# Performance work log

Hardware: AMD Instinct MI355X
Metric: run time of the kernel (lower is better)

The kernel has to match this reference:

```python
import jax, jax.numpy as jnp
import numpy as np


def setup_inputs() -> dict:
    key = jax.random.key(0)
    k1, k2, k3, k4, k5 = jax.random.split(key, 5)
    B, S, H, F, E = 2, 512, 1024, 3584, 8
    scale_in = 1.0 / np.sqrt(H)
    scale_ff = 1.0 / np.sqrt(F)
    return {
        "hidden_states": jax.random.normal(k1, (B, S, H), dtype=jnp.float32),
        "gate_w": jax.random.normal(k2, (E, H), dtype=jnp.float32) * scale_in,
        "w1": jax.random.normal(k3, (E, F, H), dtype=jnp.float32) * scale_in,
        "w2": jax.random.normal(k4, (E, H, F), dtype=jnp.float32) * scale_ff,
        "w3": jax.random.normal(k5, (E, F, H), dtype=jnp.float32) * scale_in,
    }


TOP_K = 2


def reference(hidden_states, gate_w, w1, w2, w3):
    B, S, H = hidden_states.shape
    E = gate_w.shape[0]
    x = hidden_states.reshape(B * S, H)  # [T, H]
    T = x.shape[0]

    # Router: softmax in fp32, top-2 selection, renormalize selected weights.
    router_logits = x @ gate_w.T  # [T, E]
    probs = jax.nn.softmax(router_logits.astype(jnp.float32), axis=-1)
    top_vals, top_idx = jax.lax.top_k(probs, TOP_K)  # [T, K]
    top_vals = top_vals / jnp.sum(top_vals, axis=-1, keepdims=True)
    top_vals = top_vals.astype(x.dtype)

    # Dense routing-weight matrix [T, E]: weight if selected else 0
    # (equivalent to the one-hot expert_mask + index_add combine).
    dense_w = jnp.zeros((T, E), dtype=x.dtype).at[
        jnp.arange(T)[:, None], top_idx
    ].add(top_vals)

    # Expert SwiGLU MLPs, batched over the expert axis.
    h1 = jnp.einsum("th,efh->etf", x, w1)  # [E, T, F]
    h3 = jnp.einsum("th,efh->etf", x, w3)  # [E, T, F]
    y = jnp.einsum("etf,ehf->eth", jax.nn.silu(h1) * h3, w2)  # [E, T, H]

    # Weighted combine across experts.
    out = jnp.einsum("eth,te->th", y, dense_w)  # [T, H]
    return out.reshape(B, S, H), router_logits
```

## Files before the change

kernel.cpp:

```cpp
#include <hip/hip_runtime.h>
#include <hip/hip_bf16.h>

typedef __bf16 v8bf __attribute__((ext_vector_type(8)));
typedef __bf16 v4bf __attribute__((ext_vector_type(4)));
typedef float  f32x4 __attribute__((ext_vector_type(4)));
typedef unsigned int u32;

#define NTOK 1024
#define HDIM 1024
#define FDIM 3584
#define NEXP 8
#define NPAIR 2048
#define MAXT 16
#define KSPLIT2 4
#define KPER2 (FDIM / KSPLIT2)

#define OFF_COUNTS   0
#define OFF_OFFSETS  64
#define OFF_NT1      128
#define OFF_T1E      192
#define OFF_T1M      320
#define OFF_TOKIDX   2048
#define OFF_TOKWT    (2048 + 4*NPAIR)
#define OFF_PAIRTOK  (OFF_TOKWT + 4*NPAIR)
#define OFF_PAIRWT   (OFF_PAIRTOK + 4*NPAIR)
#define OFF_SLOTOF   (OFF_PAIRWT + 4*NPAIR)
#define OFF_XB       65536
#define OFF_ACT      (OFF_XB + 2ull*NTOK*HDIM)
#define OFF_Y        (OFF_ACT + 2ull*NPAIR*FDIM)
#define YSTRIDE      ((size_t)NPAIR * HDIM)

static __device__ inline v4bf cvt4(float4 f) {
    v4bf r;
    r[0] = (__bf16)f.x; r[1] = (__bf16)f.y; r[2] = (__bf16)f.z; r[3] = (__bf16)f.w;
    return r;
}

static __device__ inline v8bf pack8(f32x4 lo, f32x4 hi) {
    v8bf r;
    r[0] = (__bf16)lo[0]; r[1] = (__bf16)lo[1]; r[2] = (__bf16)lo[2]; r[3] = (__bf16)lo[3];
    r[4] = (__bf16)hi[0]; r[5] = (__bf16)hi[1]; r[6] = (__bf16)hi[2]; r[7] = (__bf16)hi[3];
    return r;
}

#define FENCE() asm volatile("" ::: "memory")
#define BARRIER() do { FENCE(); __builtin_amdgcn_s_barrier(); FENCE(); } while (0)
#define WAITVM0() asm volatile("s_waitcnt vmcnt(0)" ::: "memory")
#define WAITLGKM0() asm volatile("s_waitcnt lgkmcnt(0)" ::: "memory")

#define DMA16(SRC, DST) \
    __builtin_amdgcn_global_load_lds((const __attribute__((address_space(1))) u32*)(SRC), \
                                     (__attribute__((address_space(3))) u32*)(DST), 16, 0, 0)

__global__ __launch_bounds__(256) void moe_cvtx(const float* __restrict__ x,
                                                __bf16* __restrict__ xb)
{
    const size_t i = ((size_t)blockIdx.x * 256 + threadIdx.x) * 4;
    float4 v = *(const float4*)(x + i);
    *(v4bf*)(xb + i) = cvt4(v);
}

__global__ __launch_bounds__(256) void moe_router(
    const float* __restrict__ x, const float* __restrict__ gw,
    float* __restrict__ logits, int* __restrict__ counts,
    int* __restrict__ tok_idx, float* __restrict__ tok_wt)
{
    const int lane = threadIdx.x & 63;
    const int wv = threadIdx.x >> 6;
    const int t = blockIdx.x * 4 + wv;
    const float* xr = x + (size_t)t * HDIM;

    float acc[NEXP];
#pragma unroll
    for (int e = 0; e < NEXP; ++e) acc[e] = 0.f;
#pragma unroll
    for (int j = 0; j < 4; ++j) {
        int h = lane * 4 + j * 256;
        float4 xv = *(const float4*)(xr + h);
#pragma unroll
        for (int e = 0; e < NEXP; ++e) {
            float4 g = *(const float4*)(gw + e * HDIM + h);
            acc[e] += xv.x * g.x + xv.y * g.y + xv.z * g.z + xv.w * g.w;
        }
    }
#pragma unroll
    for (int e = 0; e < NEXP; ++e) {
#pragma unroll
        for (int s = 32; s > 0; s >>= 1) acc[e] += __shfl_xor(acc[e], s);
    }
    if (lane == 0) {
#pragma unroll
        for (int e = 0; e < NEXP; ++e) logits[t * NEXP + e] = acc[e];
        int i0 = 0;
#pragma unroll
        for (int e = 1; e < NEXP; ++e) if (acc[e] > acc[i0]) i0 = e;
        int i1 = (i0 == 0) ? 1 : 0;
#pragma unroll
        for (int e = 0; e < NEXP; ++e) if (e != i0 && acc[e] > acc[i1]) i1 = e;
        float w0 = 1.f / (1.f + expf(acc[i1] - acc[i0]));
        float w1 = 1.f - w0;
        tok_idx[2 * t] = i0; tok_idx[2 * t + 1] = i1;
        tok_wt[2 * t] = w0;  tok_wt[2 * t + 1] = w1;
        atomicAdd(&counts[i0], 1);
        atomicAdd(&counts[i1], 1);
    }
}

__global__ void moe_scatter(const int* __restrict__ counts, const int* __restrict__ tok_idx,
                            const float* __restrict__ tok_wt, int* __restrict__ offsets,
                            int* __restrict__ pair_token, float* __restrict__ pair_wt,
                            int* __restrict__ slot_of,
                            int* __restrict__ t1e, int* __restrict__ t1m, int* __restrict__ nt1)
{
    __shared__ int cur[NEXP];
    const int tid = threadIdx.x;
    if (tid == 0) {
        int run = 0, n1 = 0;
        for (int e = 0; e < NEXP; ++e) {
            offsets[e] = run; cur[e] = run;
            for (int m0 = 0; m0 < counts[e]; m0 += 256) { t1e[n1] = e; t1m[n1] = m0; ++n1; }
            run += counts[e];
        }
        *nt1 = n1;
    }
    __syncthreads();
    for (int p = tid; p < 2 * NTOK; p += blockDim.x) {
        int e = tok_idx[p];
        int s = atomicAdd(&cur[e], 1);
        pair_token[s] = p >> 1;
        pair_wt[s] = tok_wt[p];
        slot_of[p] = s;
    }
}

__global__ __launch_bounds__(256, 2) void moe_gemm1(
    const __bf16* __restrict__ xb, const float* __restrict__ w1g,
    const float* __restrict__ w3g, const int* __restrict__ counts,
    const int* __restrict__ offsets, const int* __restrict__ pair_token,
    const int* __restrict__ t1e, const int* __restrict__ t1m,
    const int* __restrict__ nt1,
    __bf16* __restrict__ act)
{
    const int ty = blockIdx.y;
    if (ty >= *nt1) return;
    const int e = t1e[ty];
    const int m0 = t1m[ty];
    const int Me = counts[e];
    const int rows = min(256, Me - m0);
    const int slot0 = offsets[e] + m0;
    const int n0 = blockIdx.x * 32;

    __shared__ __align__(16) __bf16 As[256 * 64];
    __shared__ __align__(16) float  B1s[32 * 64];
    __shared__ __align__(16) float  B3s[32 * 64];

    const int tid = threadIdx.x;
    const int lane = tid & 63;
    const int wv = tid >> 6;
    const int ln4 = lane >> 4;
    const int lr = lane & 15;
    const int wm = (wv >> 1) * 128;
    const int wn = (wv & 1) * 16;

    f32x4 acc1[8], acc3[8];
#pragma unroll
    for (int i = 0; i < 8; ++i) {
        acc1[i] = (f32x4){0.f, 0.f, 0.f, 0.f};
        acc3[i] = (f32x4){0.f, 0.f, 0.f, 0.f};
    }

    const char* asrc[8];
#pragma unroll
    for (int i = 0; i < 8; ++i) {
        int c = i * 256 + tid;
        int r = c >> 3;
        int rr = (r < rows) ? r : 0;
        int sj = (c & 7) ^ (r & 7);
        asrc[i] = (const char*)(xb + (size_t)pair_token[slot0 + rr] * HDIM) + sj * 16;
    }
    const char* bsrc[2];
#pragma unroll
    for (int i = 0; i < 2; ++i) {
        int c = i * 256 + tid;
        int r = c >> 4;
        int sj = (c & 15) ^ (r & 15);
        bsrc[i] = (const char*)(w1g + ((size_t)e * FDIM + n0 + r) * HDIM) + sj * 16;
    }
    const ptrdiff_t d31b = (const char*)w3g - (const char*)w1g;

#define DMA_ALL1(K0) do { \
    _Pragma("unroll") \
    for (int i = 0; i < 8; ++i) \
        DMA16(asrc[i] + (size_t)(K0) * 128, (char*)As + (i * 256 + wv * 64) * 16); \
    _Pragma("unroll") \
    for (int i = 0; i < 2; ++i) { \
        DMA16(bsrc[i] + (size_t)(K0) * 256,        (char*)B1s + (i * 256 + wv * 64) * 16); \
        DMA16(bsrc[i] + d31b + (size_t)(K0) * 256, (char*)B3s + (i * 256 + wv * 64) * 16); \
    } } while (0)

    int abase[8], axor[8];
#pragma unroll
    for (int i = 0; i < 8; ++i) {
        int row = wm + i * 16 + lr;
        abase[i] = row * 128;
        axor[i] = (row & 7) << 4;
    }
    int bbase, bxor;
    {
        int row = wn + lr;
        bbase = row * 256;
        bxor = (row & 15) << 4;
    }

#define CMP1() do { \
    _Pragma("unroll") \
    for (int ksub = 0; ksub < 2; ++ksub) { \
        int in0 = ksub * 128 + ln4 * 32; \
        v8bf b1f = pack8(*(const f32x4*)((const char*)B1s + bbase + ((in0) ^ bxor)), \
                         *(const f32x4*)((const char*)B1s + bbase + ((in0 + 16) ^ bxor))); \
        v8bf b3f = pack8(*(const f32x4*)((const char*)B3s + bbase + ((in0) ^ bxor)), \
                         *(const f32x4*)((const char*)B3s + bbase + ((in0 + 16) ^ bxor))); \
        _Pragma("unroll") \
        for (int mi = 0; mi < 8; ++mi) { \
            v8bf af = *(const v8bf*)((const char*)As + abase[mi] + ((ksub * 64 + ln4 * 16) ^ axor[mi])); \
            acc1[mi] = __builtin_amdgcn_mfma_f32_16x16x32_bf16(af, b1f, acc1[mi], 0, 0, 0); \
            acc3[mi] = __builtin_amdgcn_mfma_f32_16x16x32_bf16(af, b3f, acc3[mi], 0, 0, 0); \
        } } } while (0)

    DMA_ALL1(0);
    for (int ks = 0; ks < HDIM / 64; ++ks) {
        WAITVM0();
        BARRIER();
        CMP1();
        WAITLGKM0();
        BARRIER();
        if (ks + 1 < HDIM / 64) DMA_ALL1(ks + 1);
    }
#undef DMA_ALL1
#undef CMP1

    const int rj = ln4 * 4;
#pragma unroll
    for (int mi = 0; mi < 8; ++mi) {
#pragma unroll
        for (int j = 0; j < 4; ++j) {
            int rm = wm + mi * 16 + rj + j;
            if (rm < rows) {
                size_t rowoff = (size_t)(slot0 + rm) * FDIM + n0 + wn;
                float h1 = acc1[mi][j];
                float h3 = acc3[mi][j];
                float sv = (h1 / (1.f + __expf(-h1))) * h3;
                act[rowoff + lr] = (__bf16)sv;
            }
        }
    }
}

__global__ __launch_bounds__(256, 2) void moe_gemm2(
    const __bf16* __restrict__ act, const float* __restrict__ w2g,
    const int* __restrict__ counts, const int* __restrict__ offsets,
    const int* __restrict__ t1e, const int* __restrict__ t1m,
    const int* __restrict__ nt1,
    float* __restrict__ y)
{
    const int ty = blockIdx.y;
    if (ty >= *nt1) return;
    const int e = t1e[ty];
    const int m0 = t1m[ty];
    const int Me = counts[e];
    const int rows = min(256, Me - m0);
    const int slot0 = offsets[e] + m0;
    const int n0 = blockIdx.x * 64;
    const int kz = blockIdx.z;
    float* yout = y + (size_t)kz * YSTRIDE;
    const size_t kbase = (size_t)kz * KPER2;

    __shared__ __align__(16) __bf16 As[256 * 64];
    __shared__ __align__(16) float  Bs[64 * 64];

    const int tid = threadIdx.x;
    const int lane = tid & 63;
    const int wv = tid >> 6;
    const int ln4 = lane >> 4;
    const int lr = lane & 15;
    const int wm = (wv >> 1) * 128;
    const int wn = (wv & 1) * 32;

    f32x4 acc[8][2];
#pragma unroll
    for (int i = 0; i < 8; ++i)
#pragma unroll
        for (int j = 0; j < 2; ++j) acc[i][j] = (f32x4){0.f, 0.f, 0.f, 0.f};

    const char* asrc[8];
#pragma unroll
    for (int i = 0; i < 8; ++i) {
        int c = i * 256 + tid;
        int r = c >> 3;
        int rr = (r < rows) ? r : 0;
        int sj = (c & 7) ^ (r & 7);
        asrc[i] = (const char*)(act + (size_t)(slot0 + rr) * FDIM + kbase) + sj * 16;
    }
    const char* bsrc[4];
#pragma unroll
    for (int i = 0; i < 4; ++i) {
        int c = i * 256 + tid;
        int r = c >> 4;
        int sj = (c & 15) ^ (r & 15);
        bsrc[i] = (const char*)(w2g + ((size_t)e * HDIM + n0 + r) * FDIM + kbase) + sj * 16;
    }

#define DMA_ALL2(K0) do { \
    _Pragma("unroll") \
    for (int i = 0; i < 8; ++i) \
        DMA16(asrc[i] + (size_t)(K0) * 128, (char*)As + (i * 256 + wv * 64) * 16); \
    _Pragma("unroll") \
    for (int i = 0; i < 4; ++i) \
        DMA16(bsrc[i] + (size_t)(K0) * 256, (char*)Bs + (i * 256 + wv * 64) * 16); \
    } while (0)

    int abase[8], axor[8];
#pragma unroll
    for (int i = 0; i < 8; ++i) {
        int row = wm + i * 16 + lr;
        abase[i] = row * 128;
        axor[i] = (row & 7) << 4;
    }
    int bbase[2], bxor[2];
#pragma unroll
    for (int i = 0; i < 2; ++i) {
        int row = wn + i * 16 + lr;
        bbase[i] = row * 256;
        bxor[i] = (row & 15) << 4;
    }

#define CMP2() do { \
    _Pragma("unroll") \
    for (int ksub = 0; ksub < 2; ++ksub) { \
        v8bf bf[2]; \
        _Pragma("unroll") \
        for (int ni = 0; ni < 2; ++ni) { \
            int in0 = ksub * 128 + ln4 * 32; \
            bf[ni] = pack8(*(const f32x4*)((const char*)Bs + bbase[ni] + ((in0) ^ bxor[ni])), \
                           *(const f32x4*)((const char*)Bs + bbase[ni] + ((in0 + 16) ^ bxor[ni]))); } \
        _Pragma("unroll") \
        for (int mi = 0; mi < 8; ++mi) { \
            v8bf af = *(const v8bf*)((const char*)As + abase[mi] + ((ksub * 64 + ln4 * 16) ^ axor[mi])); \
            _Pragma("unroll") \
            for (int ni = 0; ni < 2; ++ni) \
                acc[mi][ni] = __builtin_amdgcn_mfma_f32_16x16x32_bf16(af, bf[ni], acc[mi][ni], 0, 0, 0); \
        } } } while (0)

    DMA_ALL2(0);
    for (int ks = 0; ks < KPER2 / 64; ++ks) {
        WAITVM0();
        BARRIER();
        CMP2();
        WAITLGKM0();
        BARRIER();
        if (ks + 1 < KPER2 / 64) DMA_ALL2(ks + 1);
    }
#undef DMA_ALL2
#undef CMP2

    const int rj = ln4 * 4;
#pragma unroll
    for (int mi = 0; mi < 8; ++mi) {
#pragma unroll
        for (int j = 0; j < 4; ++j) {
            int rm = wm + mi * 16 + rj + j;
            if (rm < rows) {
                size_t rowoff = (size_t)(slot0 + rm) * HDIM + n0 + wn;
#pragma unroll
                for (int ni = 0; ni < 2; ++ni)
                    yout[rowoff + ni * 16 + lr] = acc[mi][ni][j];
            }
        }
    }
}

__global__ __launch_bounds__(256) void moe_combine(
    const float* __restrict__ y, const int* __restrict__ slot_of,
    const float* __restrict__ pair_wt, float* __restrict__ out)
{
    const int t = blockIdx.x;
    const int tid = threadIdx.x;
    const int s0 = slot_of[2 * t];
    const int s1 = slot_of[2 * t + 1];
    const float w0 = pair_wt[s0];
    const float w1 = pair_wt[s1];
    float4 a = {0.f, 0.f, 0.f, 0.f}, b = {0.f, 0.f, 0.f, 0.f};
#pragma unroll
    for (int k = 0; k < KSPLIT2; ++k) {
        const float4 ak = *(const float4*)(y + k * YSTRIDE + (size_t)s0 * HDIM + tid * 4);
        const float4 bk = *(const float4*)(y + k * YSTRIDE + (size_t)s1 * HDIM + tid * 4);
        a.x += ak.x; a.y += ak.y; a.z += ak.z; a.w += ak.w;
        b.x += bk.x; b.y += bk.y; b.z += bk.z; b.w += bk.w;
    }
    float4 o;
    o.x = w0 * a.x + w1 * b.x;
    o.y = w0 * a.y + w1 * b.y;
    o.z = w0 * a.z + w1 * b.z;
    o.w = w0 * a.w + w1 * b.w;
    *(float4*)(out + (size_t)t * HDIM + tid * 4) = o;
}

extern "C" void kernel_launch(void* const* d_in, const int* in_sizes, int n_in,
                              void* d_out, int out_size, void* d_ws, size_t ws_size,
                              hipStream_t stream) {
    const float* x   = (const float*)d_in[0];
    const float* gw  = (const float*)d_in[1];
    const float* w1  = (const float*)d_in[2];
    const float* w2  = (const float*)d_in[3];
    const float* w3  = (const float*)d_in[4];

    float* out    = (float*)d_out;
    float* logits = out + (size_t)NTOK * HDIM;

    char* ws = (char*)d_ws;
    int*    counts     = (int*)(ws + OFF_COUNTS);
    int*    offsets    = (int*)(ws + OFF_OFFSETS);
    int*    nt1        = (int*)(ws + OFF_NT1);
    int*    t1e        = (int*)(ws + OFF_T1E);
    int*    t1m        = (int*)(ws + OFF_T1M);
    int*    tok_idx    = (int*)(ws + OFF_TOKIDX);
    float*  tok_wt     = (float*)(ws + OFF_TOKWT);
    int*    pair_token = (int*)(ws + OFF_PAIRTOK);
    float*  pair_wt    = (float*)(ws + OFF_PAIRWT);
    int*    slot_of    = (int*)(ws + OFF_SLOTOF);
    __bf16* xb         = (__bf16*)(ws + OFF_XB);
    __bf16* act        = (__bf16*)(ws + OFF_ACT);
    float*  yb         = (float*)(ws + OFF_Y);

    hipMemsetAsync(counts, 0, 64, stream);

    moe_cvtx<<<dim3(NTOK * HDIM / 1024), dim3(256), 0, stream>>>(x, xb);
    moe_router<<<dim3(NTOK / 4), dim3(256), 0, stream>>>(x, gw, logits, counts, tok_idx, tok_wt);
    moe_scatter<<<dim3(1), dim3(256), 0, stream>>>(counts, tok_idx, tok_wt, offsets,
                                                   pair_token, pair_wt, slot_of,
                                                   t1e, t1m, nt1);
    moe_gemm1<<<dim3(FDIM / 32, MAXT), dim3(256), 0, stream>>>(
        xb, w1, w3, counts, offsets, pair_token, t1e, t1m, nt1, act);
    moe_gemm2<<<dim3(HDIM / 64, MAXT, KSPLIT2), dim3(256), 0, stream>>>(
        act, w2, counts, offsets, t1e, t1m, nt1, yb);
    moe_combine<<<dim3(NTOK), dim3(256), 0, stream>>>(yb, slot_of, pair_wt, out);
}
```

Measured before the change: 192.1 us.

## Double-buffer MoE GEMM smem tiles and shrink M tiles to 128 rows

Both expert GEMMs now keep two shared-memory buffers and prefetch two K-steps ahead. They wait with partial vmcnt counts, so global-to-LDS DMA overlaps the MFMA work, and they raise wave priority around the compute. Token tiles shrink from 256 to 128 rows, which doubles the maximum tile count. GEMM2 uses 32-wide N tiles, a K-split of 2 and a higher occupancy bound, so more blocks are in flight and latency is better hidden. The risk is that the fp32 expert weights are re-read by twice as many M tiles, which adds memory traffic unless L2 absorbs it.

```diff
diff --git a/kernel.cpp b/kernel.cpp
--- a/kernel.cpp
+++ b/kernel.cpp
@@ -11,9 +11,11 @@
 #define FDIM 3584
 #define NEXP 8
 #define NPAIR 2048
-#define MAXT 16
-#define KSPLIT2 4
+#define MAXT 32
+#define KSPLIT2 2
 #define KPER2 (FDIM / KSPLIT2)
+#define NS1 (HDIM / 64)
+#define NS2 (KPER2 / 64)
 
 #define OFF_COUNTS   0
 #define OFF_OFFSETS  64
@@ -45,7 +47,7 @@
 
 #define FENCE() asm volatile("" ::: "memory")
 #define BARRIER() do { FENCE(); __builtin_amdgcn_s_barrier(); FENCE(); } while (0)
-#define WAITVM0() asm volatile("s_waitcnt vmcnt(0)" ::: "memory")
+#define WAITVM(N) asm volatile("s_waitcnt vmcnt(" #N ")" ::: "memory")
 #define WAITLGKM0() asm volatile("s_waitcnt lgkmcnt(0)" ::: "memory")
 
 #define DMA16(SRC, DST) \
@@ -118,7 +120,7 @@
         int run = 0, n1 = 0;
         for (int e = 0; e < NEXP; ++e) {
             offsets[e] = run; cur[e] = run;
-            for (int m0 = 0; m0 < counts[e]; m0 += 256) { t1e[n1] = e; t1m[n1] = m0; ++n1; }
+            for (int m0 = 0; m0 < counts[e]; m0 += 128) { t1e[n1] = e; t1m[n1] = m0; ++n1; }
             run += counts[e];
         }
         *nt1 = n1;
@@ -146,32 +148,32 @@
     const int e = t1e[ty];
     const int m0 = t1m[ty];
     const int Me = counts[e];
-    const int rows = min(256, Me - m0);
+    const int rows = min(128, Me - m0);
     const int slot0 = offsets[e] + m0;
     const int n0 = blockIdx.x * 32;
 
-    __shared__ __align__(16) __bf16 As[256 * 64];
-    __shared__ __align__(16) float  B1s[32 * 64];
-    __shared__ __align__(16) float  B3s[32 * 64];
+    __shared__ __align__(16) __bf16 As[2][128 * 64];
+    __shared__ __align__(16) float  B1s[2][32 * 64];
+    __shared__ __align__(16) float  B3s[2][32 * 64];
 
     const int tid = threadIdx.x;
     const int lane = tid & 63;
     const int wv = tid >> 6;
     const int ln4 = lane >> 4;
     const int lr = lane & 15;
-    const int wm = (wv >> 1) * 128;
+    const int wm = (wv >> 1) * 64;
     const int wn = (wv & 1) * 16;
 
-    f32x4 acc1[8], acc3[8];
-#pragma unroll
-    for (int i = 0; i < 8; ++i) {
+    f32x4 acc1[4], acc3[4];
+#pragma unroll
+    for (int i = 0; i < 4; ++i) {
         acc1[i] = (f32x4){0.f, 0.f, 0.f, 0.f};
         acc3[i] = (f32x4){0.f, 0.f, 0.f, 0.f};
     }
 
-    const char* asrc[8];
-#pragma unroll
-    for (int i = 0; i < 8; ++i) {
+    const char* asrc[4];
+#pragma unroll
+    for (int i = 0; i < 4; ++i) {
         int c = i * 256 + tid;
         int r = c >> 3;
         int rr = (r < rows) ? r : 0;
@@ -188,19 +190,19 @@
     }
     const ptrdiff_t d31b = (const char*)w3g - (const char*)w1g;
 
-#define DMA_ALL1(K0) do { \
-    _Pragma("unroll") \
-    for (int i = 0; i < 8; ++i) \
-        DMA16(asrc[i] + (size_t)(K0) * 128, (char*)As + (i * 256 + wv * 64) * 16); \
+#define DMA1(BUF, K0) do { \
+    _Pragma("unroll") \
+    for (int i = 0; i < 4; ++i) \
+        DMA16(asrc[i] + (size_t)(K0) * 128, (char*)&As[BUF][0] + (i * 256 + wv * 64) * 16); \
     _Pragma("unroll") \
     for (int i = 0; i < 2; ++i) { \
-        DMA16(bsrc[i] + (size_t)(K0) * 256,        (char*)B1s + (i * 256 + wv * 64) * 16); \
-        DMA16(bsrc[i] + d31b + (size_t)(K0) * 256, (char*)B3s + (i * 256 + wv * 64) * 16); \
+        DMA16(bsrc[i] + (size_t)(K0) * 256,        (char*)&B1s[BUF][0] + (i * 256 + wv * 64) * 16); \
+        DMA16(bsrc[i] + d31b + (size_t)(K0) * 256, (char*)&B3s[BUF][0] + (i * 256 + wv * 64) * 16); \
     } } while (0)
 
-    int abase[8], axor[8];
-#pragma unroll
-    for (int i = 0; i < 8; ++i) {
+    int abase[4], axor[4];
+#pragma unroll
+    for (int i = 0; i < 4; ++i) {
         int row = wm + i * 16 + lr;
         abase[i] = row * 128;
         axor[i] = (row & 7) << 4;
@@ -212,51 +214,58 @@
         bxor = (row & 15) << 4;
     }
 
-#define CMP1() do { \
+#define CMP1(BUF) do { \
+    const char* Ab = (const char*)&As[BUF][0]; \
+    const char* B1b = (const char*)&B1s[BUF][0]; \
+    const char* B3b = (const char*)&B3s[BUF][0]; \
+    __builtin_amdgcn_s_setprio(1); \
     _Pragma("unroll") \
     for (int ksub = 0; ksub < 2; ++ksub) { \
         int in0 = ksub * 128 + ln4 * 32; \
-        v8bf b1f = pack8(*(const f32x4*)((const char*)B1s + bbase + ((in0) ^ bxor)), \
-                         *(const f32x4*)((const char*)B1s + bbase + ((in0 + 16) ^ bxor))); \
-        v8bf b3f = pack8(*(const f32x4*)((const char*)B3s + bbase + ((in0) ^ bxor)), \
-                         *(const f32x4*)((const char*)B3s + bbase + ((in0 + 16) ^ bxor))); \
+        v8bf b1f = pack8(*(const f32x4*)(B1b + bbase + ((in0) ^ bxor)), \
+                         *(const f32x4*)(B1b + bbase + ((in0 + 16) ^ bxor))); \
+        v8bf b3f = pack8(*(const f32x4*)(B3b + bbase + ((in0) ^ bxor)), \
+                         *(const f32x4*)(B3b + bbase + ((in0 + 16) ^ bxor))); \
         _Pragma("unroll") \
-        for (int mi = 0; mi < 8; ++mi) { \
-            v8bf af = *(const v8bf*)((const char*)As + abase[mi] + ((ksub * 64 + ln4 * 16) ^ axor[mi])); \
+        for (int mi = 0; mi < 4; ++mi) { \
+            v8bf af = *(const v8bf*)(Ab + abase[mi] + ((ksub * 64 + ln4 * 16) ^ axor[mi])); \
             acc1[mi] = __builtin_amdgcn_mfma_f32_16x16x32_bf16(af, b1f, acc1[mi], 0, 0, 0); \
             acc3[mi] = __builtin_amdgcn_mfma_f32_16x16x32_bf16(af, b3f, acc3[mi], 0, 0, 0); \
-        } } } while (0)
-
-    DMA_ALL1(0);
-    for (int ks = 0; ks < HDIM / 64; ++ks) {
-        WAITVM0();
+        } } \
+    __builtin_amdgcn_s_setprio(0); \
+    } while (0)
+
+    DMA1(0, 0);
+    DMA1(1, 1);
+    for (int ks = 0; ks < NS1; ++ks) {
+        if (ks < NS1 - 1) WAITVM(8);
+        else              WAITVM(0);
         BARRIER();
-        CMP1();
+        CMP1(ks & 1);
         WAITLGKM0();
         BARRIER();
-        if (ks + 1 < HDIM / 64) DMA_ALL1(ks + 1);
-    }
-#undef DMA_ALL1
+        if (ks + 2 < NS1) DMA1(ks & 1, ks + 2);
+    }
+#undef DMA1
 #undef CMP1
 
     const int rj = ln4 * 4;
 #pragma unroll
-    for (int mi = 0; mi < 8; ++mi) {
+    for (int mi = 0; mi < 4; ++mi) {
 #pragma unroll
         for (int j = 0; j < 4; ++j) {
             int rm = wm + mi * 16 + rj + j;
             if (rm < rows) {
-                size_t rowoff = (size_t)(slot0 + rm) * FDIM + n0 + wn;
                 float h1 = acc1[mi][j];
                 float h3 = acc3[mi][j];
                 float sv = (h1 / (1.f + __expf(-h1))) * h3;
-                act[rowoff + lr] = (__bf16)sv;
+                act[(size_t)(slot0 + rm) * FDIM + n0 + wn + lr] = (__bf16)sv;
             }
         }
     }
 }
 
-__global__ __launch_bounds__(256, 2) void moe_gemm2(
+__global__ __launch_bounds__(256, 3) void moe_gemm2(
     const __bf16* __restrict__ act, const float* __restrict__ w2g,
     const int* __restrict__ counts, const int* __restrict__ offsets,
     const int* __restrict__ t1e, const int* __restrict__ t1m,
@@ -268,112 +277,108 @@
     const int e = t1e[ty];
     const int m0 = t1m[ty];
     const int Me = counts[e];
-    const int rows = min(256, Me - m0);
+    const int rows = min(128, Me - m0);
     const int slot0 = offsets[e] + m0;
-    const int n0 = blockIdx.x * 64;
+    const int n0 = blockIdx.x * 32;
     const int kz = blockIdx.z;
     float* yout = y + (size_t)kz * YSTRIDE;
     const size_t kbase = (size_t)kz * KPER2;
 
-    __shared__ __align__(16) __bf16 As[256 * 64];
-    __shared__ __align__(16) float  Bs[64 * 64];
+    __shared__ __align__(16) __bf16 As[2][128 * 64];
+    __shared__ __align__(16) float  Bs[2][32 * 64];
 
     const int tid = threadIdx.x;
     const int lane = tid & 63;
     const int wv = tid >> 6;
     const int ln4 = lane >> 4;
     const int lr = lane & 15;
-    const int wm = (wv >> 1) * 128;
-    const int wn = (wv & 1) * 32;
-
-    f32x4 acc[8][2];
-#pragma unroll
-    for (int i = 0; i < 8; ++i)
-#pragma unroll
-        for (int j = 0; j < 2; ++j) acc[i][j] = (f32x4){0.f, 0.f, 0.f, 0.f};
-
-    const char* asrc[8];
-#pragma unroll
-    for (int i = 0; i < 8; ++i) {
+    const int wm = (wv >> 1) * 64;
+    const int wn = (wv & 1) * 16;
+
+    f32x4 acc[4];
+#pragma unroll
+    for (int i = 0; i < 4; ++i) acc[i] = (f32x4){0.f, 0.f, 0.f, 0.f};
+
+    const char* asrc[4];
+#pragma unroll
+    for (int i = 0; i < 4; ++i) {
         int c = i * 256 + tid;
         int r = c >> 3;
         int rr = (r < rows) ? r : 0;
         int sj = (c & 7) ^ (r & 7);
         asrc[i] = (const char*)(act + (size_t)(slot0 + rr) * FDIM + kbase) + sj * 16;
     }
-    const char* bsrc[4];
-#pragma unroll
-    for (int i = 0; i < 4; ++i) {
+    const char* bsrc[2];
+#pragma unroll
+    for (int i = 0; i < 2; ++i) {
         int c = i * 256 + tid;
         int r = c >> 4;
         int sj = (c & 15) ^ (r & 15);
         bsrc[i] = (const char*)(w2g + ((size_t)e * HDIM + n0 + r) * FDIM + kbase) + sj * 16;
     }
 
-#define DMA_ALL2(K0) do { \
-    _Pragma("unroll") \
-    for (int i = 0; i < 8; ++i) \
-        DMA16(asrc[i] + (size_t)(K0) * 128, (char*)As + (i * 256 + wv * 64) * 16); \
+#define DMA2(BUF, K0) do { \
     _Pragma("unroll") \
     for (int i = 0; i < 4; ++i) \
-        DMA16(bsrc[i] + (size_t)(K0) * 256, (char*)Bs + (i * 256 + wv * 64) * 16); \
+        DMA16(asrc[i] + (size_t)(K0) * 128, (char*)&As[BUF][0] + (i * 256 + wv * 64) * 16); \
+    _Pragma("unroll") \
+    for (int i = 0; i < 2; ++i) \
+        DMA16(bsrc[i] + (size_t)(K0) * 256, (char*)&Bs[BUF][0] + (i * 256 + wv * 64) * 16); \
     } while (0)
 
-    int abase[8], axor[8];
-#pragma unroll
-    for (int i = 0; i < 8; ++i) {
+    int abase[4], axor[4];
+#pragma unroll
+    for (int i = 0; i < 4; ++i) {
         int row = wm + i * 16 + lr;
         abase[i] = row * 128;
         axor[i] = (row & 7) << 4;
     }
-    int bbase[2], bxor[2];
-#pragma unroll
-    for (int i = 0; i < 2; ++i) {
-        int row = wn + i * 16 + lr;
-        bbase[i] = row * 256;
-        bxor[i] = (row & 15) << 4;
-    }
-
-#define CMP2() do { \
+    int bbase, bxor;
+    {
+        int row = wn + lr;
+        bbase = row * 256;
+        bxor = (row & 15) << 4;
+    }
+
+#define CMP2(BUF) do { \
+    const char* Ab = (const char*)&As[BUF][0]; \
+    const char* Bb = (const char*)&Bs[BUF][0]; \
+    __builtin_amdgcn_s_setprio(1); \
     _Pragma("unroll") \
     for (int ksub = 0; ksub < 2; ++ksub) { \
-        v8bf bf[2]; \
+        int in0 = ksub * 128 + ln4 * 32; \
+        v8bf bf = pack8(*(const f32x4*)(Bb + bbase + ((in0) ^ bxor)), \
+                        *(const f32x4*)(Bb + bbase + ((in0 + 16) ^ bxor))); \
         _Pragma("unroll") \
-        for (int ni = 0; ni < 2; ++ni) { \
-            int in0 = ksub * 128 + ln4 * 32; \
-            bf[ni] = pack8(*(const f32x4*)((const char*)Bs + bbase[ni] + ((in0) ^ bxor[ni])), \
-                           *(const f32x4*)((const char*)Bs + bbase[ni] + ((in0 + 16) ^ bxor[ni]))); } \
-        _Pragma("unroll") \
-        for (int mi = 0; mi < 8; ++mi) { \
-            v8bf af = *(const v8bf*)((const char*)As + abase[mi] + ((ksub * 64 + ln4 * 16) ^ axor[mi])); \
-            _Pragma("unroll") \
-            for (int ni = 0; ni < 2; ++ni) \
-                acc[mi][ni] = __builtin_amdgcn_mfma_f32_16x16x32_bf16(af, bf[ni], acc[mi][ni], 0, 0, 0); \
-        } } } while (0)
-
-    DMA_ALL2(0);
-    for (int ks = 0; ks < KPER2 / 64; ++ks) {
-        WAITVM0();
+        for (int mi = 0; mi < 4; ++mi) { \
+            v8bf af = *(const v8bf*)(Ab + abase[mi] + ((ksub * 64 + ln4 * 16) ^ axor[mi])); \
+            acc[mi] = __builtin_amdgcn_mfma_f32_16x16x32_bf16(af, bf, acc[mi], 0, 0, 0); \
+        } } \
+    __builtin_amdgcn_s_setprio(0); \
+    } while (0)
+
+    DMA2(0, 0);
+    DMA2(1, 1);
+    for (int ks = 0; ks < NS2; ++ks) {
+        if (ks < NS2 - 1) WAITVM(6);
+        else              WAITVM(0);
         BARRIER();
-        CMP2();
+        CMP2(ks & 1);
         WAITLGKM0();
         BARRIER();
-        if (ks + 1 < KPER2 / 64) DMA_ALL2(ks + 1);
-    }
-#undef DMA_ALL2
+        if (ks + 2 < NS2) DMA2(ks & 1, ks + 2);
+    }
+#undef DMA2
 #undef CMP2
 
     const int rj = ln4 * 4;
 #pragma unroll
-    for (int mi = 0; mi < 8; ++mi) {
+    for (int mi = 0; mi < 4; ++mi) {
 #pragma unroll
         for (int j = 0; j < 4; ++j) {
             int rm = wm + mi * 16 + rj + j;
             if (rm < rows) {
-                size_t rowoff = (size_t)(slot0 + rm) * HDIM + n0 + wn;
-#pragma unroll
-                for (int ni = 0; ni < 2; ++ni)
-                    yout[rowoff + ni * 16 + lr] = acc[mi][ni][j];
+                yout[(size_t)(slot0 + rm) * HDIM + n0 + wn + lr] = acc[mi][j];
             }
         }
     }
@@ -441,7 +446,7 @@
                                                    t1e, t1m, nt1);
     moe_gemm1<<<dim3(FDIM / 32, MAXT), dim3(256), 0, stream>>>(
         xb, w1, w3, counts, offsets, pair_token, t1e, t1m, nt1, act);
-    moe_gemm2<<<dim3(HDIM / 64, MAXT, KSPLIT2), dim3(256), 0, stream>>>(
+    moe_gemm2<<<dim3(HDIM / 32, MAXT, KSPLIT2), dim3(256), 0, stream>>>(
         act, w2, counts, offsets, t1e, t1m, nt1, yb);
     moe_combine<<<dim3(NTOK), dim3(256), 0, stream>>>(yb, slot_of, pair_wt, out);
 }
```

Result: slower. 212.1 us (+10.4%).

## Fuse MoE combine into gemm2 via atomics, smaller M tiles, XCD-aware block swizzle

Applied to the files above, without the earlier changes.

Drops the separate combine kernel and the fp32 split-K partial buffer. gemm2 now multiplies each result by its routing weight and atomically adds it straight into the zeroed output. gemm2 uses 128-row M tiles with a separate tile list, occupancy of 4, and loads all A and B fragments before the MFMAs. Both GEMMs use a 1D grid with an 8-way XCD swizzle so blocks that share weights land on the same XCD. This removes a large intermediate write and read plus one launch, at the cost of fp32 atomic contention, non-deterministic summation order, and an extra memset of the output.

```diff
diff --git a/kernel.cpp b/kernel.cpp
--- a/kernel.cpp
+++ b/kernel.cpp
@@ -11,15 +11,28 @@
 #define FDIM 3584
 #define NEXP 8
 #define NPAIR 2048
-#define MAXT 16
+#define MAXT1 16
+#define MAXT2 32
 #define KSPLIT2 4
 #define KPER2 (FDIM / KSPLIT2)
+#define NS1 (HDIM / 64)
+#define NS2 (KPER2 / 64)
+
+#define G1_NB (FDIM / 32)
+#define G1_NWG (G1_NB * MAXT1)
+#define G1_CPX (G1_NWG / 8)
+#define G2_NB (HDIM / 64)
+#define G2_NWG (G2_NB * KSPLIT2 * MAXT2)
+#define G2_CPX (G2_NWG / 8)
 
 #define OFF_COUNTS   0
 #define OFF_OFFSETS  64
 #define OFF_NT1      128
+#define OFF_NT2      132
 #define OFF_T1E      192
 #define OFF_T1M      320
+#define OFF_T2E      448
+#define OFF_T2M      704
 #define OFF_TOKIDX   2048
 #define OFF_TOKWT    (2048 + 4*NPAIR)
 #define OFF_PAIRTOK  (OFF_TOKWT + 4*NPAIR)
@@ -27,8 +40,6 @@
 #define OFF_SLOTOF   (OFF_PAIRWT + 4*NPAIR)
 #define OFF_XB       65536
 #define OFF_ACT      (OFF_XB + 2ull*NTOK*HDIM)
-#define OFF_Y        (OFF_ACT + 2ull*NPAIR*FDIM)
-#define YSTRIDE      ((size_t)NPAIR * HDIM)
 
 static __device__ inline v4bf cvt4(float4 f) {
     v4bf r;
@@ -110,18 +121,20 @@
                             const float* __restrict__ tok_wt, int* __restrict__ offsets,
                             int* __restrict__ pair_token, float* __restrict__ pair_wt,
                             int* __restrict__ slot_of,
-                            int* __restrict__ t1e, int* __restrict__ t1m, int* __restrict__ nt1)
+                            int* __restrict__ t1e, int* __restrict__ t1m, int* __restrict__ nt1,
+                            int* __restrict__ t2e, int* __restrict__ t2m, int* __restrict__ nt2)
 {
     __shared__ int cur[NEXP];
     const int tid = threadIdx.x;
     if (tid == 0) {
-        int run = 0, n1 = 0;
+        int run = 0, n1 = 0, n2 = 0;
         for (int e = 0; e < NEXP; ++e) {
             offsets[e] = run; cur[e] = run;
             for (int m0 = 0; m0 < counts[e]; m0 += 256) { t1e[n1] = e; t1m[n1] = m0; ++n1; }
+            for (int m0 = 0; m0 < counts[e]; m0 += 128) { t2e[n2] = e; t2m[n2] = m0; ++n2; }
             run += counts[e];
         }
-        *nt1 = n1;
+        *nt1 = n1; *nt2 = n2;
     }
     __syncthreads();
     for (int p = tid; p < 2 * NTOK; p += blockDim.x) {
@@ -141,14 +154,17 @@
     const int* __restrict__ nt1,
     __bf16* __restrict__ act)
 {
-    const int ty = blockIdx.y;
+    const int g = blockIdx.x;
+    const int swz = (g & 7) * G1_CPX + (g >> 3);
+    const int ty = swz % MAXT1;
+    const int nb = swz / MAXT1;
     if (ty >= *nt1) return;
     const int e = t1e[ty];
     const int m0 = t1m[ty];
     const int Me = counts[e];
     const int rows = min(256, Me - m0);
     const int slot0 = offsets[e] + m0;
-    const int n0 = blockIdx.x * 32;
+    const int n0 = nb * 32;
 
     __shared__ __align__(16) __bf16 As[256 * 64];
     __shared__ __align__(16) float  B1s[32 * 64];
@@ -228,13 +244,13 @@
         } } } while (0)
 
     DMA_ALL1(0);
-    for (int ks = 0; ks < HDIM / 64; ++ks) {
+    for (int ks = 0; ks < NS1; ++ks) {
         WAITVM0();
         BARRIER();
         CMP1();
         WAITLGKM0();
         BARRIER();
-        if (ks + 1 < HDIM / 64) DMA_ALL1(ks + 1);
+        if (ks + 1 < NS1) DMA_ALL1(ks + 1);
     }
 #undef DMA_ALL1
 #undef CMP1
@@ -256,26 +272,30 @@
     }
 }
 
-__global__ __launch_bounds__(256, 2) void moe_gemm2(
+__global__ __launch_bounds__(256, 4) void moe_gemm2(
     const __bf16* __restrict__ act, const float* __restrict__ w2g,
     const int* __restrict__ counts, const int* __restrict__ offsets,
-    const int* __restrict__ t1e, const int* __restrict__ t1m,
-    const int* __restrict__ nt1,
-    float* __restrict__ y)
+    const int* __restrict__ pair_token, const float* __restrict__ pair_wt,
+    const int* __restrict__ t2e, const int* __restrict__ t2m,
+    const int* __restrict__ nt2,
+    float* __restrict__ out)
 {
-    const int ty = blockIdx.y;
-    if (ty >= *nt1) return;
-    const int e = t1e[ty];
-    const int m0 = t1m[ty];
+    const int g = blockIdx.x;
+    const int swz = (g & 7) * G2_CPX + (g >> 3);
+    const int ty = swz % MAXT2;
+    const int rest = swz / MAXT2;
+    const int kz = rest % KSPLIT2;
+    const int nb = rest / KSPLIT2;
+    if (ty >= *nt2) return;
+    const int e = t2e[ty];
+    const int m0 = t2m[ty];
     const int Me = counts[e];
-    const int rows = min(256, Me - m0);
+    const int rows = min(128, Me - m0);
     const int slot0 = offsets[e] + m0;
-    const int n0 = blockIdx.x * 64;
-    const int kz = blockIdx.z;
-    float* yout = y + (size_t)kz * YSTRIDE;
+    const int n0 = nb * 64;
     const size_t kbase = (size_t)kz * KPER2;
 
-    __shared__ __align__(16) __bf16 As[256 * 64];
+    __shared__ __align__(16) __bf16 As[128 * 64];
     __shared__ __align__(16) float  Bs[64 * 64];
 
     const int tid = threadIdx.x;
@@ -283,18 +303,18 @@
     const int wv = tid >> 6;
     const int ln4 = lane >> 4;
     const int lr = lane & 15;
-    const int wm = (wv >> 1) * 128;
+    const int wm = (wv >> 1) * 64;
     const int wn = (wv & 1) * 32;
 
-    f32x4 acc[8][2];
-#pragma unroll
-    for (int i = 0; i < 8; ++i)
+    f32x4 acc[4][2];
+#pragma unroll
+    for (int i = 0; i < 4; ++i)
 #pragma unroll
         for (int j = 0; j < 2; ++j) acc[i][j] = (f32x4){0.f, 0.f, 0.f, 0.f};
 
-    const char* asrc[8];
-#pragma unroll
-    for (int i = 0; i < 8; ++i) {
+    const char* asrc[4];
+#pragma unroll
+    for (int i = 0; i < 4; ++i) {
         int c = i * 256 + tid;
         int r = c >> 3;
         int rr = (r < rows) ? r : 0;
@@ -310,18 +330,15 @@
         bsrc[i] = (const char*)(w2g + ((size_t)e * HDIM + n0 + r) * FDIM + kbase) + sj * 16;
     }
 
-#define DMA_ALL2(K0) do { \
-    _Pragma("unroll") \
-    for (int i = 0; i < 8; ++i) \
+#define DMA_ALL2(K0) do { _Pragma("unroll") \
+    for (int i = 0; i < 4; ++i) { \
         DMA16(asrc[i] + (size_t)(K0) * 128, (char*)As + (i * 256 + wv * 64) * 16); \
-    _Pragma("unroll") \
-    for (int i = 0; i < 4; ++i) \
         DMA16(bsrc[i] + (size_t)(K0) * 256, (char*)Bs + (i * 256 + wv * 64) * 16); \
-    } while (0)
-
-    int abase[8], axor[8];
-#pragma unroll
-    for (int i = 0; i < 8; ++i) {
+    } } while (0)
+
+    int abase[4], axor[4];
+#pragma unroll
+    for (int i = 0; i < 4; ++i) {
         int row = wm + i * 16 + lr;
         abase[i] = row * 128;
         axor[i] = (row & 7) << 4;
@@ -335,74 +352,54 @@
     }
 
 #define CMP2() do { \
-    _Pragma("unroll") \
-    for (int ksub = 0; ksub < 2; ++ksub) { \
-        v8bf bf[2]; \
-        _Pragma("unroll") \
-        for (int ni = 0; ni < 2; ++ni) { \
-            int in0 = ksub * 128 + ln4 * 32; \
-            bf[ni] = pack8(*(const f32x4*)((const char*)Bs + bbase[ni] + ((in0) ^ bxor[ni])), \
-                           *(const f32x4*)((const char*)Bs + bbase[ni] + ((in0 + 16) ^ bxor[ni]))); } \
-        _Pragma("unroll") \
-        for (int mi = 0; mi < 8; ++mi) { \
-            v8bf af = *(const v8bf*)((const char*)As + abase[mi] + ((ksub * 64 + ln4 * 16) ^ axor[mi])); \
-            _Pragma("unroll") \
-            for (int ni = 0; ni < 2; ++ni) \
-                acc[mi][ni] = __builtin_amdgcn_mfma_f32_16x16x32_bf16(af, bf[ni], acc[mi][ni], 0, 0, 0); \
-        } } } while (0)
+    v8bf af[4][2], bf[2][2]; \
+    _Pragma("unroll") \
+    for (int mi = 0; mi < 4; ++mi) { _Pragma("unroll") \
+        for (int ks = 0; ks < 2; ++ks) \
+            af[mi][ks] = *(const v8bf*)((const char*)As + abase[mi] + ((ks * 64 + ln4 * 16) ^ axor[mi])); } \
+    _Pragma("unroll") \
+    for (int ni = 0; ni < 2; ++ni) { _Pragma("unroll") \
+        for (int ks = 0; ks < 2; ++ks) { \
+            int in0 = ks * 128 + ln4 * 32; \
+            f32x4 lo = *(const f32x4*)((const char*)Bs + bbase[ni] + ((in0) ^ bxor[ni])); \
+            f32x4 hi = *(const f32x4*)((const char*)Bs + bbase[ni] + ((in0 + 16) ^ bxor[ni])); \
+            bf[ni][ks] = pack8(lo, hi); } } \
+    _Pragma("unroll") \
+    for (int mi = 0; mi < 4; ++mi) { _Pragma("unroll") \
+        for (int ni = 0; ni < 2; ++ni) { _Pragma("unroll") \
+            for (int ks = 0; ks < 2; ++ks) \
+                acc[mi][ni] = __builtin_amdgcn_mfma_f32_16x16x32_bf16(af[mi][ks], bf[ni][ks], acc[mi][ni], 0, 0, 0); } } \
+    } while (0)
 
     DMA_ALL2(0);
-    for (int ks = 0; ks < KPER2 / 64; ++ks) {
+    for (int ks = 0; ks < NS2; ++ks) {
         WAITVM0();
         BARRIER();
         CMP2();
         WAITLGKM0();
         BARRIER();
-        if (ks + 1 < KPER2 / 64) DMA_ALL2(ks + 1);
+        if (ks + 1 < NS2) DMA_ALL2(ks + 1);
     }
 #undef DMA_ALL2
 #undef CMP2
 
     const int rj = ln4 * 4;
 #pragma unroll
-    for (int mi = 0; mi < 8; ++mi) {
+    for (int mi = 0; mi < 4; ++mi) {
 #pragma unroll
         for (int j = 0; j < 4; ++j) {
             int rm = wm + mi * 16 + rj + j;
             if (rm < rows) {
-                size_t rowoff = (size_t)(slot0 + rm) * HDIM + n0 + wn;
+                int slot = slot0 + rm;
+                int tok = pair_token[slot];
+                float w = pair_wt[slot];
+                size_t rowoff = (size_t)tok * HDIM + n0 + wn;
 #pragma unroll
                 for (int ni = 0; ni < 2; ++ni)
-                    yout[rowoff + ni * 16 + lr] = acc[mi][ni][j];
+                    atomicAdd(&out[rowoff + ni * 16 + lr], w * acc[mi][ni][j]);
             }
         }
     }
-}
-
-__global__ __launch_bounds__(256) void moe_combine(
-    const float* __restrict__ y, const int* __restrict__ slot_of,
-    const float* __restrict__ pair_wt, float* __restrict__ out)
-{
-    const int t = blockIdx.x;
-    const int tid = threadIdx.x;
-    const int s0 = slot_of[2 * t];
-    const int s1 = slot_of[2 * t + 1];
-    const float w0 = pair_wt[s0];
-    const float w1 = pair_wt[s1];
-    float4 a = {0.f, 0.f, 0.f, 0.f}, b = {0.f, 0.f, 0.f, 0.f};
-#pragma unroll
-    for (int k = 0; k < KSPLIT2; ++k) {
-        const float4 ak = *(const float4*)(y + k * YSTRIDE + (size_t)s0 * HDIM + tid * 4);
-        const float4 bk = *(const float4*)(y + k * YSTRIDE + (size_t)s1 * HDIM + tid * 4);
-        a.x += ak.x; a.y += ak.y; a.z += ak.z; a.w += ak.w;
-        b.x += bk.x; b.y += bk.y; b.z += bk.z; b.w += bk.w;
-    }
-    float4 o;
-    o.x = w0 * a.x + w1 * b.x;
-    o.y = w0 * a.y + w1 * b.y;
-    o.z = w0 * a.z + w1 * b.z;
-    o.w = w0 * a.w + w1 * b.w;
-    *(float4*)(out + (size_t)t * HDIM + tid * 4) = o;
 }
 
 extern "C" void kernel_launch(void* const* d_in, const int* in_sizes, int n_in,
@@ -421,8 +418,11 @@
     int*    counts     = (int*)(ws + OFF_COUNTS);
     int*    offsets    = (int*)(ws + OFF_OFFSETS);
     int*    nt1        = (int*)(ws + OFF_NT1);
+    int*    nt2        = (int*)(ws + OFF_NT2);
     int*    t1e        = (int*)(ws + OFF_T1E);
     int*    t1m        = (int*)(ws + OFF_T1M);
+    int*    t2e        = (int*)(ws + OFF_T2E);
+    int*    t2m        = (int*)(ws + OFF_T2M);
     int*    tok_idx    = (int*)(ws + OFF_TOKIDX);
     float*  tok_wt     = (float*)(ws + OFF_TOKWT);
     int*    pair_token = (int*)(ws + OFF_PAIRTOK);
@@ -430,18 +430,17 @@
     int*    slot_of    = (int*)(ws + OFF_SLOTOF);
     __bf16* xb         = (__bf16*)(ws + OFF_XB);
     __bf16* act        = (__bf16*)(ws + OFF_ACT);
-    float*  yb         = (float*)(ws + OFF_Y);
 
     hipMemsetAsync(counts, 0, 64, stream);
+    hipMemsetAsync(out, 0, (size_t)NTOK * HDIM * sizeof(float), stream);
 
     moe_cvtx<<<dim3(NTOK * HDIM / 1024), dim3(256), 0, stream>>>(x, xb);
     moe_router<<<dim3(NTOK / 4), dim3(256), 0, stream>>>(x, gw, logits, counts, tok_idx, tok_wt);
     moe_scatter<<<dim3(1), dim3(256), 0, stream>>>(counts, tok_idx, tok_wt, offsets,
                                                    pair_token, pair_wt, slot_of,
-                                                   t1e, t1m, nt1);
-    moe_gemm1<<<dim3(FDIM / 32, MAXT), dim3(256), 0, stream>>>(
+                                                   t1e, t1m, nt1, t2e, t2m, nt2);
+    moe_gemm1<<<dim3(G1_NWG), dim3(256), 0, stream>>>(
         xb, w1, w3, counts, offsets, pair_token, t1e, t1m, nt1, act);
-    moe_gemm2<<<dim3(HDIM / 64, MAXT, KSPLIT2), dim3(256), 0, stream>>>(
-        act, w2, counts, offsets, t1e, t1m, nt1, yb);
-    moe_combine<<<dim3(NTOK), dim3(256), 0, stream>>>(yb, slot_of, pair_wt, out);
-}
+    moe_gemm2<<<dim3(G2_NWG), dim3(256), 0, stream>>>(
+        act, w2, counts, offsets, pair_token, pair_wt, t2e, t2m, nt2, out);
+}
```

Result: slower. 207.3 us (+7.9%).
